# Kernel optimization log

Measured on AMD Instinct MI355X. Metric: run time of the kernel, lower is better.

Reference implementation:

```python
import jax, jax.numpy as jnp
import numpy as np

EMBED = 1024
HEADS = 16
HEAD_DIM = EMBED // HEADS
FFN = 4096
BSZ = 2
CHUNK = 128
NCHUNK = 16
REG_LEN = CHUNK * NCHUNK   # 2048
SUM_LEN = NCHUNK           # 1 summary token per chunk
NEG = -1e9


def _layer_norm(x, g, b, eps=1e-5):
    mu = x.mean(-1, keepdims=True)
    var = ((x - mu) ** 2).mean(-1, keepdims=True)
    return (x - mu) * jax.lax.rsqrt(var + eps) * g + b


def _build_mask(reg_chunk_ranges, sum_len, reg_len):
    # True = attention allowed. Museformer hierarchical scheme:
    #   rr: reg token attends reg tokens of its OWN chunk, causally
    #   rs: reg token attends summary tokens of STRICTLY EARLIER chunks
    #   sr: summary token of chunk c attends reg tokens of chunk c
    #   ss: causal among summary tokens
    bsz = reg_chunk_ranges.shape[0]
    starts = reg_chunk_ranges[:, :, 0]                       # [B, C]
    t = jnp.arange(reg_len)
    chunk_id = (t[None, :, None] >= starts[:, None, :]).sum(-1) - 1   # [B, R]
    sum_chunk = jnp.arange(sum_len)                          # [S]
    rr = (chunk_id[:, :, None] == chunk_id[:, None, :]) & (t[None, :, None] >= t[None, None, :])
    rs = sum_chunk[None, None, :] < chunk_id[:, :, None]     # [B, R, S]
    sr = chunk_id[:, None, :] == sum_chunk[None, :, None]    # [B, S, R]
    ss = jnp.broadcast_to(sum_chunk[:, None] >= sum_chunk[None, :], (bsz, sum_len, sum_len))
    top = jnp.concatenate([ss, sr], axis=2)
    bot = jnp.concatenate([rs, rr], axis=2)
    return jnp.concatenate([top, bot], axis=1)               # [B, S+R, S+R]


def _forward(x, w_q, w_k, w_v, w_o,
             ln_sa_sum_g, ln_sa_sum_b, ln_sa_reg_g, ln_sa_reg_b,
             sum_fc1_w, sum_fc1_b, sum_fc2_w, sum_fc2_b,
             reg_fc1_w, reg_fc1_b, reg_fc2_w, reg_fc2_b,
             ln_f_sum_g, ln_f_sum_b, ln_f_reg_g, ln_f_reg_b,
             reg_chunk_ranges, sum_len, reg_len):
    bsz, total, d = x.shape
    # --- self-attention block (pre-norm, separate LN for sum/reg parts) ---
    hs = _layer_norm(x[:, :sum_len], ln_sa_sum_g, ln_sa_sum_b)
    hr = _layer_norm(x[:, sum_len:], ln_sa_reg_g, ln_sa_reg_b)
    h = jnp.concatenate([hs, hr], axis=1)
    q = (h @ w_q.T).reshape(bsz, total, HEADS, HEAD_DIM)
    k = (h @ w_k.T).reshape(bsz, total, HEADS, HEAD_DIM)
    v = (h @ w_v.T).reshape(bsz, total, HEADS, HEAD_DIM)
    scores = jnp.einsum('bqhd,bkhd->bhqk', q, k) * (HEAD_DIM ** -0.5)
    mask = _build_mask(reg_chunk_ranges, sum_len, reg_len)   # [B, T, T] bool
    scores = jnp.where(mask[:, None], scores, NEG)
    attn = jax.nn.softmax(scores, axis=-1)
    ctx = jnp.einsum('bhqk,bkhd->bqhd', attn, v).reshape(bsz, total, d)
    x = x + ctx @ w_o.T
    # --- FFN block (pre-norm, separate LN/FFN for sum/reg parts) ---
    fs = _layer_norm(x[:, :sum_len], ln_f_sum_g, ln_f_sum_b)
    fs = jax.nn.relu(fs @ sum_fc1_w.T + sum_fc1_b) @ sum_fc2_w.T + sum_fc2_b
    fr = _layer_norm(x[:, sum_len:], ln_f_reg_g, ln_f_reg_b)
    fr = jax.nn.relu(fr @ reg_fc1_w.T + reg_fc1_b) @ reg_fc2_w.T + reg_fc2_b
    return x + jnp.concatenate([fs, fr], axis=1)


def setup_inputs() -> dict:
    key = jax.random.key(0)
    ks = jax.random.split(key, 12)
    s = 0.02
    total = SUM_LEN + REG_LEN
    starts = (np.arange(NCHUNK) * CHUNK).astype(np.int32)
    ranges = np.stack([starts, starts + CHUNK], axis=-1)     # [C, 2]
    reg_chunk_ranges = jnp.asarray(np.broadcast_to(ranges, (BSZ, NCHUNK, 2)).copy())
    d = dict(
        x=jax.random.normal(ks[0], (BSZ, total, EMBED), jnp.float32),
        w_q=jax.random.normal(ks[1], (EMBED, EMBED), jnp.float32) * s,
        w_k=jax.random.normal(ks[2], (EMBED, EMBED), jnp.float32) * s,
        w_v=jax.random.normal(ks[3], (EMBED, EMBED), jnp.float32) * s,
        w_o=jax.random.normal(ks[4], (EMBED, EMBED), jnp.float32) * s,
        ln_sa_sum_g=jnp.ones((EMBED,)), ln_sa_sum_b=jnp.zeros((EMBED,)),
        ln_sa_reg_g=jnp.ones((EMBED,)), ln_sa_reg_b=jnp.zeros((EMBED,)),
        sum_fc1_w=jax.random.normal(ks[5], (FFN, EMBED), jnp.float32) * s,
        sum_fc1_b=jnp.zeros((FFN,)),
        sum_fc2_w=jax.random.normal(ks[6], (EMBED, FFN), jnp.float32) * s,
        sum_fc2_b=jnp.zeros((EMBED,)),
        reg_fc1_w=jax.random.normal(ks[7], (FFN, EMBED), jnp.float32) * s,
        reg_fc1_b=jnp.zeros((FFN,)),
        reg_fc2_w=jax.random.normal(ks[8], (EMBED, FFN), jnp.float32) * s,
        reg_fc2_b=jnp.zeros((EMBED,)),
        ln_f_sum_g=jnp.ones((EMBED,)), ln_f_sum_b=jnp.zeros((EMBED,)),
        ln_f_reg_g=jnp.ones((EMBED,)), ln_f_reg_b=jnp.zeros((EMBED,)),
        reg_chunk_ranges=reg_chunk_ranges,
        sum_len=SUM_LEN,
        reg_len=REG_LEN,
    )
    return d


def reference(x, w_q, w_k, w_v, w_o,
              ln_sa_sum_g, ln_sa_sum_b, ln_sa_reg_g, ln_sa_reg_b,
              sum_fc1_w, sum_fc1_b, sum_fc2_w, sum_fc2_b,
              reg_fc1_w, reg_fc1_b, reg_fc2_w, reg_fc2_b,
              ln_f_sum_g, ln_f_sum_b, ln_f_reg_g, ln_f_reg_b,
              reg_chunk_ranges, sum_len, reg_len):
    return _forward(x, w_q, w_k, w_v, w_o,
                    ln_sa_sum_g, ln_sa_sum_b, ln_sa_reg_g, ln_sa_reg_b,
                    sum_fc1_w, sum_fc1_b, sum_fc2_w, sum_fc2_b,
                    reg_fc1_w, reg_fc1_b, reg_fc2_w, reg_fc2_b,
                    ln_f_sum_g, ln_f_sum_b, ln_f_reg_g, ln_f_reg_b,
                    reg_chunk_ranges, sum_len, reg_len)
```

## Files before the change

kernel.cpp:

```cpp
#include <hip/hip_runtime.h>
#include <stdint.h>

typedef __attribute__((ext_vector_type(8))) short short8;
typedef __attribute__((ext_vector_type(4))) float f32x4;

__device__ __forceinline__ float bf2f(short s) {
    union { unsigned u; float f; } c;
    c.u = ((unsigned)(unsigned short)s) << 16;
    return c.f;
}
__device__ __forceinline__ short f2bf(float f) {
    union { float f; unsigned u; } c; c.f = f;
    unsigned u = c.u + 0x7fffu + ((c.u >> 16) & 1u);
    return (short)(u >> 16);
}
__device__ __forceinline__ void gll16(const short* g, short* l) {
    __builtin_amdgcn_global_load_lds(
        (const __attribute__((address_space(1))) unsigned int*)g,
        (__attribute__((address_space(3))) unsigned int*)l, 16, 0, 0);
}

__global__ __launch_bounds__(256) void cvt_w(
    const float* __restrict__ wq, const float* __restrict__ wk,
    const float* __restrict__ wv, const float* __restrict__ wo,
    const float* __restrict__ f1s, const float* __restrict__ f2s,
    const float* __restrict__ f1r, const float* __restrict__ f2r,
    short* __restrict__ dst)
{
    size_t i = ((size_t)blockIdx.x * 256 + threadIdx.x) * 4;
    const float* src; size_t off;
    if (i < 4194304) {
        int seg = (int)(i >> 20);
        src = seg == 0 ? wq : seg == 1 ? wk : seg == 2 ? wv : wo;
        off = i & 1048575;
    } else {
        size_t ii = i - 4194304;
        int seg = (int)(ii >> 22);
        src = seg == 0 ? f1s : seg == 1 ? f2s : seg == 2 ? f1r : f2r;
        off = ii & 4194303;
    }
    float4 v = *(const float4*)(src + off);
    short4 o;
    o.x = f2bf(v.x); o.y = f2bf(v.y); o.z = f2bf(v.z); o.w = f2bf(v.w);
    *(short4*)(dst + i) = o;
}

template<int PHASE>
__global__ __launch_bounds__(256) void ln_k(
    const float* __restrict__ xin,
    const float* __restrict__ g_sum, const float* __restrict__ b_sum,
    const float* __restrict__ g_reg, const float* __restrict__ b_reg,
    short* __restrict__ out_all, short* __restrict__ out_s, short* __restrict__ out_r)
{
    int row = blockIdx.x;
    int b = row / 2064, t = row - b * 2064;
    int tid = threadIdx.x;
    const float* xr = xin + (size_t)row * 1024;
    float4 v = *(const float4*)(xr + tid * 4);
    float s = v.x + v.y + v.z + v.w;
#pragma unroll
    for (int off = 1; off < 64; off <<= 1) s += __shfl_xor(s, off);
    __shared__ float red[8];
    if ((tid & 63) == 0) red[tid >> 6] = s;
    __syncthreads();
    float mu = (red[0] + red[1] + red[2] + red[3]) * (1.0f / 1024.0f);
    float a0 = v.x - mu, a1 = v.y - mu, a2 = v.z - mu, a3 = v.w - mu;
    float qq = a0 * a0 + a1 * a1 + a2 * a2 + a3 * a3;
#pragma unroll
    for (int off = 1; off < 64; off <<= 1) qq += __shfl_xor(qq, off);
    if ((tid & 63) == 0) red[4 + (tid >> 6)] = qq;
    __syncthreads();
    float var = (red[4] + red[5] + red[6] + red[7]) * (1.0f / 1024.0f);
    float rs = rsqrtf(var + 1e-5f);
    const float* g  = (t < 16) ? g_sum : g_reg;
    const float* be = (t < 16) ? b_sum : b_reg;
    int c = tid * 4;
    short4 o;
    o.x = f2bf(a0 * rs * g[c]     + be[c]);
    o.y = f2bf(a1 * rs * g[c + 1] + be[c + 1]);
    o.z = f2bf(a2 * rs * g[c + 2] + be[c + 2]);
    o.w = f2bf(a3 * rs * g[c + 3] + be[c + 3]);
    short* dst;
    if (PHASE == 0) dst = out_all + (size_t)row * 1024;
    else dst = (t < 16) ? (out_s + ((size_t)b * 16 + t) * 1024)
                        : (out_r + ((size_t)b * 2048 + (t - 16)) * 1024);
    *(short4*)(dst + c) = o;
}

template<int MODE>
__global__ __launch_bounds__(256) void gemm_bt(
    const short* __restrict__ A, int M, int K, int klen,
    const short* __restrict__ B0, const short* __restrict__ B1, const short* __restrict__ B2,
    const float* __restrict__ bias,
    void* __restrict__ o0, void* __restrict__ o1, void* __restrict__ o2, int seg)
{
    const int tid = threadIdx.x;
    const int w = tid >> 6, l = tid & 63;
    const int lr = l & 15, lh = l >> 4;
    const int m0 = blockIdx.x * 128;
    int ntile = blockIdx.y, nsel = 0;
    const short* B = B0;
    if (MODE == 0) { nsel = ntile >> 3; ntile &= 7; B = nsel == 0 ? B0 : (nsel == 1 ? B1 : B2); }
    const int n0 = ntile * 128;
    const int wr = (w >> 1) * 64, wc = (w & 1) * 64;
    const int kbase = blockIdx.z * klen;

    __shared__ __align__(16) short As[128 * 32];
    __shared__ __align__(16) short Bs[128 * 32];

    const int srow = w * 32 + (l >> 2);
    const int scol = (l & 3) * 8;
    int ar0 = m0 + srow;      if (ar0 > M - 1) ar0 = M - 1;
    int ar1 = m0 + srow + 16; if (ar1 > M - 1) ar1 = M - 1;
    const short* ga0 = A + (size_t)ar0 * K + scol;
    const short* ga1 = A + (size_t)ar1 * K + scol;
    const short* gb0 = B + (size_t)(n0 + srow) * K + scol;
    const short* gb1 = B + (size_t)(n0 + srow + 16) * K + scol;
    short* la0 = As + (w * 32) * 32;
    short* la1 = As + (w * 32 + 16) * 32;
    short* lb0 = Bs + (w * 32) * 32;
    short* lb1 = Bs + (w * 32 + 16) * 32;

    f32x4 acc[4][4];
#pragma unroll
    for (int m = 0; m < 4; ++m)
#pragma unroll
        for (int n = 0; n < 4; ++n) acc[m][n] = (f32x4){0.f, 0.f, 0.f, 0.f};

    for (int k0 = kbase; k0 < kbase + klen; k0 += 32) {
        gll16(ga0 + k0, la0);
        gll16(ga1 + k0, la1);
        gll16(gb0 + k0, lb0);
        gll16(gb1 + k0, lb1);
        __syncthreads();
        short8 af[4], bfr[4];
#pragma unroll
        for (int m = 0; m < 4; ++m)
            af[m] = *(const short8*)(As + (wr + m * 16 + lr) * 32 + lh * 8);
#pragma unroll
        for (int n = 0; n < 4; ++n)
            bfr[n] = *(const short8*)(Bs + (wc + n * 16 + lr) * 32 + lh * 8);
#pragma unroll
        for (int m = 0; m < 4; ++m)
#pragma unroll
            for (int n = 0; n < 4; ++n)
                acc[m][n] = __builtin_amdgcn_mfma_f32_16x16x32_bf16(af[m], bfr[n], acc[m][n], 0, 0, 0);
        __syncthreads();
    }

#pragma unroll
    for (int m = 0; m < 4; ++m) {
#pragma unroll
        for (int n = 0; n < 4; ++n) {
            int gc = n0 + wc + n * 16 + lr;
#pragma unroll
            for (int j = 0; j < 4; ++j) {
                int gr = m0 + wr + m * 16 + lh * 4 + j;
                if (gr >= M) continue;
                float val = acc[m][n][j];
                if (MODE == 0) {
                    short* o = (short*)(nsel == 0 ? o0 : (nsel == 1 ? o1 : o2));
                    o[(size_t)gr * 1024 + gc] = f2bf(val);
                } else if (MODE == 1) {
                    float* P = (float*)o0 + (size_t)blockIdx.z * (size_t)seg;
                    P[(size_t)gr * 1024 + gc] = val;
                } else {
                    val += bias[gc];
                    val = val > 0.f ? val : 0.f;
                    ((short*)o0)[(size_t)gr * 4096 + gc] = f2bf(val);
                }
            }
        }
    }
}

__global__ __launch_bounds__(256) void reduce_wo(
    const float* __restrict__ x, const float* __restrict__ P, float* __restrict__ x1)
{
    size_t i = ((size_t)blockIdx.x * 256 + threadIdx.x) * 4;
    float4 a  = *(const float4*)(x + i);
    float4 p0 = *(const float4*)(P + i);
    float4 p1 = *(const float4*)(P + i + 4227072);
    float4 o;
    o.x = a.x + p0.x + p1.x; o.y = a.y + p0.y + p1.y;
    o.z = a.z + p0.z + p1.z; o.w = a.w + p0.w + p1.w;
    *(float4*)(x1 + i) = o;
}

__global__ __launch_bounds__(256) void reduce_f2reg(
    const float* __restrict__ x1, const float* __restrict__ P,
    const float* __restrict__ bias, float* __restrict__ out)
{
    size_t i = ((size_t)blockIdx.x * 256 + threadIdx.x) * 4;
    int gr = (int)(i >> 10), c = (int)(i & 1023);
    size_t g = (size_t)((gr >> 11) * 2064 + 16 + (gr & 2047)) * 1024 + c;
    float4 p0 = *(const float4*)(P + i);
    float4 p1 = *(const float4*)(P + i + 4194304);
    float4 r  = *(const float4*)(x1 + g);
    float4 bb = *(const float4*)(bias + c);
    float4 o;
    o.x = r.x + p0.x + p1.x + bb.x; o.y = r.y + p0.y + p1.y + bb.y;
    o.z = r.z + p0.z + p1.z + bb.z; o.w = r.w + p0.w + p1.w + bb.w;
    *(float4*)(out + g) = o;
}

__global__ __launch_bounds__(256) void reduce_f2sum(
    const float* __restrict__ x1, const float* __restrict__ P,
    const float* __restrict__ bias, float* __restrict__ out)
{
    int i = (blockIdx.x * 256 + threadIdx.x) * 4;
    int gr = i >> 10, c = i & 1023;
    size_t g = (size_t)((gr >> 4) * 2064 + (gr & 15)) * 1024 + c;
    float4 r  = *(const float4*)(x1 + g);
    float4 bb = *(const float4*)(bias + c);
    float ox = r.x + bb.x, oy = r.y + bb.y, oz = r.z + bb.z, ow = r.w + bb.w;
#pragma unroll
    for (int s = 0; s < 16; ++s) {
        float4 p = *(const float4*)(P + s * 32768 + i);
        ox += p.x; oy += p.y; oz += p.z; ow += p.w;
    }
    float4 o; o.x = ox; o.y = oy; o.z = oz; o.w = ow;
    *(float4*)(out + g) = o;
}

__global__ __launch_bounds__(256) void attn_reg(
    const short* __restrict__ q, const short* __restrict__ k,
    const short* __restrict__ v, short* __restrict__ ctx)
{
    __shared__ __align__(16) short Pl[128 * 168];
    __shared__ __align__(16) short Vt[64 * 168];
    short* Kl = Pl;

    const int tid = threadIdx.x;
    const int w = tid >> 6, l = tid & 63, lr = l & 15, lh = l >> 4;
    const int c = blockIdx.x, h = blockIdx.y, b = blockIdx.z;
    const int hc = h * 64;
    const size_t rowq0 = (size_t)b * 2064 + 16 + (size_t)c * 128;

    for (int ch = tid; ch < 1152; ch += 256) {
        int row = ch >> 3, kk = (ch & 7) << 3;
        size_t grow = (row < 16) ? ((size_t)b * 2064 + row) : (rowq0 + row - 16);
        *(int4*)(Kl + row * 72 + kk) = *(const int4*)(k + grow * 1024 + hc + kk);
    }
    for (int ch = tid; ch < 1152; ch += 256) {
        int j = ch % 144, db = ch / 144;
        size_t grow = (j < 16) ? ((size_t)b * 2064 + j) : (rowq0 + j - 16);
        short8 dv = *(const short8*)(v + grow * 1024 + hc + db * 8);
#pragma unroll
        for (int i = 0; i < 8; ++i) Vt[(db * 8 + i) * 168 + j] = dv[i];
    }
    for (int idx = tid; idx < 1024; idx += 256) {
        int d = idx >> 4, jj = 144 + (idx & 15);
        Vt[d * 168 + jj] = 0;
    }
    __syncthreads();

    short8 qf[2][2];
#pragma unroll
    for (int m = 0; m < 2; ++m) {
        size_t grow = rowq0 + w * 32 + m * 16 + lr;
#pragma unroll
        for (int ks = 0; ks < 2; ++ks)
            qf[m][ks] = *(const short8*)(q + grow * 1024 + hc + ks * 32 + lh * 8);
    }

    f32x4 s[2][9];
#pragma unroll
    for (int m = 0; m < 2; ++m)
#pragma unroll
        for (int n = 0; n < 9; ++n) s[m][n] = (f32x4){0.f, 0.f, 0.f, 0.f};
#pragma unroll
    for (int n = 0; n < 9; ++n) {
        const short* kr = Kl + (n * 16 + lr) * 72;
        short8 k0 = *(const short8*)(kr + lh * 8);
        short8 k1 = *(const short8*)(kr + 32 + lh * 8);
        s[0][n] = __builtin_amdgcn_mfma_f32_16x16x32_bf16(qf[0][0], k0, s[0][n], 0, 0, 0);
        s[0][n] = __builtin_amdgcn_mfma_f32_16x16x32_bf16(qf[0][1], k1, s[0][n], 0, 0, 0);
        s[1][n] = __builtin_amdgcn_mfma_f32_16x16x32_bf16(qf[1][0], k0, s[1][n], 0, 0, 0);
        s[1][n] = __builtin_amdgcn_mfma_f32_16x16x32_bf16(qf[1][1], k1, s[1][n], 0, 0, 0);
    }

    float inv_[2][4];
#pragma unroll
    for (int m = 0; m < 2; ++m) {
#pragma unroll
        for (int j = 0; j < 4; ++j) {
            int p = w * 32 + m * 16 + lh * 4 + j;
            float best = -1e30f;
            float e[9];
#pragma unroll
            for (int n = 0; n < 9; ++n) {
                int kk = n * 16 + lr;
                bool vis = (kk < 16) ? (kk < c) : (kk - 16 <= p);
                float val = vis ? s[m][n][j] * 0.125f : -1e30f;
                e[n] = val;
                best = fmaxf(best, val);
            }
#pragma unroll
            for (int off = 1; off < 16; off <<= 1) best = fmaxf(best, __shfl_xor(best, off));
            float sm = 0.f;
#pragma unroll
            for (int n = 0; n < 9; ++n) {
                float ex = __expf(e[n] - best);
                s[m][n][j] = ex;
                sm += ex;
            }
#pragma unroll
            for (int off = 1; off < 16; off <<= 1) sm += __shfl_xor(sm, off);
            inv_[m][j] = 1.0f / sm;
        }
    }

    __syncthreads();
#pragma unroll
    for (int m = 0; m < 2; ++m)
#pragma unroll
        for (int n = 0; n < 9; ++n)
#pragma unroll
            for (int j = 0; j < 4; ++j)
                Pl[(w * 32 + m * 16 + lh * 4 + j) * 168 + n * 16 + lr] = f2bf(s[m][n][j]);
    for (int idx = l; idx < 512; idx += 64) {
        int rr = idx >> 4, kkp = 144 + (idx & 15);
        Pl[(w * 32 + rr) * 168 + kkp] = 0;
    }
    __syncthreads();

    f32x4 dacc[2][4];
#pragma unroll
    for (int m = 0; m < 2; ++m)
#pragma unroll
        for (int n = 0; n < 4; ++n) dacc[m][n] = (f32x4){0.f, 0.f, 0.f, 0.f};
#pragma unroll
    for (int ks = 0; ks < 5; ++ks) {
        int kk0 = ks * 32;
        short8 pa[2];
#pragma unroll
        for (int m = 0; m < 2; ++m)
            pa[m] = *(const short8*)(Pl + (w * 32 + m * 16 + lr) * 168 + kk0 + lh * 8);
#pragma unroll
        for (int n = 0; n < 4; ++n) {
            short8 vb = *(const short8*)(Vt + (n * 16 + lr) * 168 + kk0 + lh * 8);
            dacc[0][n] = __builtin_amdgcn_mfma_f32_16x16x32_bf16(pa[0], vb, dacc[0][n], 0, 0, 0);
            dacc[1][n] = __builtin_amdgcn_mfma_f32_16x16x32_bf16(pa[1], vb, dacc[1][n], 0, 0, 0);
        }
    }

#pragma unroll
    for (int m = 0; m < 2; ++m)
#pragma unroll
        for (int n = 0; n < 4; ++n)
#pragma unroll
            for (int j = 0; j < 4; ++j) {
                int p = w * 32 + m * 16 + lh * 4 + j;
                ctx[(rowq0 + p) * 1024 + hc + n * 16 + lr] = f2bf(dacc[m][n][j] * inv_[m][j]);
            }
}

__global__ __launch_bounds__(64) void attn_sum(
    const short* __restrict__ q, const short* __restrict__ k,
    const short* __restrict__ v, short* __restrict__ ctx)
{
    int idx = blockIdx.x;
    int b = idx >> 8, h = (idx >> 4) & 15, s = idx & 15;
    int l = threadIdx.x;
    int hc = h * 64;
    size_t qrow = (size_t)b * 2064 + s;
    __shared__ float qv[64];
    __shared__ float pp[192];
    qv[l] = bf2f(q[qrow * 1024 + hc + l]);
    __syncthreads();
    float sc[3];
#pragma unroll
    for (int i = 0; i < 3; ++i) {
        int j = l + i * 64;
        float t = -1e30f;
        if (j < 144 && (j >= 16 || j <= s)) {
            size_t kr = (j < 16) ? ((size_t)b * 2064 + j)
                                 : ((size_t)b * 2064 + 16 + (size_t)s * 128 + (j - 16));
            const short* kp = k + kr * 1024 + hc;
            float acc = 0.f;
            for (int d = 0; d < 64; ++d) acc += qv[d] * bf2f(kp[d]);
            t = acc * 0.125f;
        }
        sc[i] = t;
    }
    float mx = fmaxf(sc[0], fmaxf(sc[1], sc[2]));
#pragma unroll
    for (int off = 1; off < 64; off <<= 1) mx = fmaxf(mx, __shfl_xor(mx, off));
    float sm = 0.f;
#pragma unroll
    for (int i = 0; i < 3; ++i) {
        float ex = (sc[i] > -1e29f) ? __expf(sc[i] - mx) : 0.f;
        pp[l + i * 64] = ex;
        sm += ex;
    }
#pragma unroll
    for (int off = 1; off < 64; off <<= 1) sm += __shfl_xor(sm, off);
    __syncthreads();
    float invs = 1.0f / sm;
    float acc = 0.f;
    for (int j = 0; j < 144; ++j) {
        float pj = pp[j];
        size_t vr = (j < 16) ? ((size_t)b * 2064 + j)
                             : ((size_t)b * 2064 + 16 + (size_t)s * 128 + (j - 16));
        acc += pj * bf2f(v[vr * 1024 + hc + l]);
    }
    ctx[qrow * 1024 + hc + l] = f2bf(acc * invs);
}

extern "C" void kernel_launch(void* const* d_in, const int* in_sizes, int n_in,
                              void* d_out, int out_size, void* d_ws, size_t ws_size,
                              hipStream_t stream) {
    const float* x    = (const float*)d_in[0];
    const float* wq   = (const float*)d_in[1];
    const float* wk   = (const float*)d_in[2];
    const float* wv   = (const float*)d_in[3];
    const float* wo   = (const float*)d_in[4];
    const float* lsg  = (const float*)d_in[5];
    const float* lsb  = (const float*)d_in[6];
    const float* lrg  = (const float*)d_in[7];
    const float* lrb  = (const float*)d_in[8];
    const float* sf1w = (const float*)d_in[9];
    const float* sf1b = (const float*)d_in[10];
    const float* sf2w = (const float*)d_in[11];
    const float* sf2b = (const float*)d_in[12];
    const float* rf1w = (const float*)d_in[13];
    const float* rf1b = (const float*)d_in[14];
    const float* rf2w = (const float*)d_in[15];
    const float* rf2b = (const float*)d_in[16];
    const float* fsg  = (const float*)d_in[17];
    const float* fsb  = (const float*)d_in[18];
    const float* frg  = (const float*)d_in[19];
    const float* frb  = (const float*)d_in[20];
    float* out = (float*)d_out;

    char* ws = (char*)d_ws;
    short* wbf   = (short*)ws;
    short* wq_b  = wbf;
    short* wk_b  = wbf + 1048576;
    short* wv_b  = wbf + 2097152;
    short* wo_b  = wbf + 3145728;
    short* f1s_b = wbf + 4194304;
    short* f2s_b = wbf + 8388608;
    short* f1r_b = wbf + 12582912;
    short* f2r_b = wbf + 16777216;
    short* h_all  = (short*)(ws + 41943040);
    short* h2_reg = h_all;
    short* h2_sum = (short*)(ws + 41943040 + 8388608);
    float* Pwo    = (float*)(ws + 41943040);
    float* Psum   = (float*)(ws + 41943040);
    short* qb   = (short*)(ws + 50397184);
    short* kb   = qb + 4227072;
    short* vb   = kb + 4227072;
    short* ctxb = vb + 4227072;
    short* f1_reg = qb;
    short* f1_sum = qb + 16777216;
    float* Pf2 = (float*)ws;
    float* x1 = (float*)(ws + 84213760);

    cvt_w<<<20480, 256, 0, stream>>>(wq, wk, wv, wo, sf1w, sf2w, rf1w, rf2w, wbf);
    ln_k<0><<<4128, 256, 0, stream>>>(x, lsg, lsb, lrg, lrb, h_all, nullptr, nullptr);
    gemm_bt<0><<<dim3(33, 24, 1), 256, 0, stream>>>(h_all, 4128, 1024, 1024,
        wq_b, wk_b, wv_b, nullptr, qb, kb, vb, 0);
    attn_reg<<<dim3(16, 16, 2), 256, 0, stream>>>(qb, kb, vb, ctxb);
    attn_sum<<<512, 64, 0, stream>>>(qb, kb, vb, ctxb);
    gemm_bt<1><<<dim3(33, 8, 2), 256, 0, stream>>>(ctxb, 4128, 1024, 512,
        wo_b, nullptr, nullptr, nullptr, Pwo, nullptr, nullptr, 4227072);
    reduce_wo<<<4128, 256, 0, stream>>>(x, Pwo, x1);
    ln_k<1><<<4128, 256, 0, stream>>>(x1, fsg, fsb, frg, frb, nullptr, h2_sum, h2_reg);
    gemm_bt<2><<<dim3(32, 32, 1), 256, 0, stream>>>(h2_reg, 4096, 1024, 1024,
        f1r_b, nullptr, nullptr, rf1b, f1_reg, nullptr, nullptr, 0);
    gemm_bt<2><<<dim3(1, 32, 1), 256, 0, stream>>>(h2_sum, 32, 1024, 1024,
        f1s_b, nullptr, nullptr, sf1b, f1_sum, nullptr, nullptr, 0);
    gemm_bt<1><<<dim3(1, 8, 16), 256, 0, stream>>>(f1_sum, 32, 4096, 256,
        f2s_b, nullptr, nullptr, nullptr, Psum, nullptr, nullptr, 32768);
    reduce_f2sum<<<32, 256, 0, stream>>>(x1, Psum, sf2b, out);
    gemm_bt<1><<<dim3(32, 8, 2), 256, 0, stream>>>(f1_reg, 4096, 4096, 2048,
        f2r_b, nullptr, nullptr, nullptr, Pf2, nullptr, nullptr, 4194304);
    reduce_f2reg<<<4096, 256, 0, stream>>>(x1, Pf2, rf2b, out);
}
```

Measured before the change: 331.8 us.

## Double-buffer GEMM LDS tiles and fuse Wo reduction into second layer norm

The GEMM kernel now keeps two LDS buffers per operand and issues the global-to-LDS loads for the next K step before computing the current one. This removes one barrier per iteration and overlaps load latency with MFMA work. The residual add of the split-K Wo partials is folded into the second layer-norm kernel, which drops a separate elementwise pass, and workspace buffers are rearranged so the reused regions do not overlap. LDS use doubles, which may lower occupancy, and the new aliasing layout must stay free of read/write conflicts.

```diff
diff --git a/kernel.cpp b/kernel.cpp
--- a/kernel.cpp
+++ b/kernel.cpp
@@ -47,7 +47,7 @@
 
 template<int PHASE>
 __global__ __launch_bounds__(256) void ln_k(
-    const float* __restrict__ xin,
+    const float* __restrict__ xin, const float* __restrict__ P, float* __restrict__ x1out,
     const float* __restrict__ g_sum, const float* __restrict__ b_sum,
     const float* __restrict__ g_reg, const float* __restrict__ b_reg,
     short* __restrict__ out_all, short* __restrict__ out_s, short* __restrict__ out_r)
@@ -55,8 +55,16 @@
     int row = blockIdx.x;
     int b = row / 2064, t = row - b * 2064;
     int tid = threadIdx.x;
-    const float* xr = xin + (size_t)row * 1024;
-    float4 v = *(const float4*)(xr + tid * 4);
+    int c = tid * 4;
+    size_t base = (size_t)row * 1024 + c;
+    float4 v = *(const float4*)(xin + base);
+    if (PHASE == 1) {
+        float4 p0 = *(const float4*)(P + base);
+        float4 p1 = *(const float4*)(P + base + 4227072);
+        v.x += p0.x + p1.x; v.y += p0.y + p1.y;
+        v.z += p0.z + p1.z; v.w += p0.w + p1.w;
+        *(float4*)(x1out + base) = v;
+    }
     float s = v.x + v.y + v.z + v.w;
 #pragma unroll
     for (int off = 1; off < 64; off <<= 1) s += __shfl_xor(s, off);
@@ -74,7 +82,6 @@
     float rs = rsqrtf(var + 1e-5f);
     const float* g  = (t < 16) ? g_sum : g_reg;
     const float* be = (t < 16) ? b_sum : b_reg;
-    int c = tid * 4;
     short4 o;
     o.x = f2bf(a0 * rs * g[c]     + be[c]);
     o.y = f2bf(a1 * rs * g[c + 1] + be[c + 1]);
@@ -105,21 +112,18 @@
     const int wr = (w >> 1) * 64, wc = (w & 1) * 64;
     const int kbase = blockIdx.z * klen;
 
-    __shared__ __align__(16) short As[128 * 32];
-    __shared__ __align__(16) short Bs[128 * 32];
+    __shared__ __align__(16) short As[2 * 4096];
+    __shared__ __align__(16) short Bs[2 * 4096];
 
     const int srow = w * 32 + (l >> 2);
     const int scol = (l & 3) * 8;
     int ar0 = m0 + srow;      if (ar0 > M - 1) ar0 = M - 1;
     int ar1 = m0 + srow + 16; if (ar1 > M - 1) ar1 = M - 1;
-    const short* ga0 = A + (size_t)ar0 * K + scol;
-    const short* ga1 = A + (size_t)ar1 * K + scol;
-    const short* gb0 = B + (size_t)(n0 + srow) * K + scol;
-    const short* gb1 = B + (size_t)(n0 + srow + 16) * K + scol;
-    short* la0 = As + (w * 32) * 32;
-    short* la1 = As + (w * 32 + 16) * 32;
-    short* lb0 = Bs + (w * 32) * 32;
-    short* lb1 = Bs + (w * 32 + 16) * 32;
+    const short* ga0 = A + (size_t)ar0 * K + scol + kbase;
+    const short* ga1 = A + (size_t)ar1 * K + scol + kbase;
+    const short* gb0 = B + (size_t)(n0 + srow) * K + scol + kbase;
+    const short* gb1 = B + (size_t)(n0 + srow + 16) * K + scol + kbase;
+    const int lofs = (w * 32) * 32;
 
     f32x4 acc[4][4];
 #pragma unroll
@@ -127,25 +131,35 @@
 #pragma unroll
         for (int n = 0; n < 4; ++n) acc[m][n] = (f32x4){0.f, 0.f, 0.f, 0.f};
 
-    for (int k0 = kbase; k0 < kbase + klen; k0 += 32) {
-        gll16(ga0 + k0, la0);
-        gll16(ga1 + k0, la1);
-        gll16(gb0 + k0, lb0);
-        gll16(gb1 + k0, lb1);
+    gll16(ga0, As + lofs);
+    gll16(ga1, As + lofs + 512);
+    gll16(gb0, Bs + lofs);
+    gll16(gb1, Bs + lofs + 512);
+
+    const int nk = klen >> 5;
+    for (int t = 0; t < nk; ++t) {
         __syncthreads();
+        const int cur = (t & 1) << 12;
+        if (t + 1 < nk) {
+            const int nb = cur ^ 4096;
+            const int k0 = (t + 1) * 32;
+            gll16(ga0 + k0, As + nb + lofs);
+            gll16(ga1 + k0, As + nb + lofs + 512);
+            gll16(gb0 + k0, Bs + nb + lofs);
+            gll16(gb1 + k0, Bs + nb + lofs + 512);
+        }
         short8 af[4], bfr[4];
 #pragma unroll
         for (int m = 0; m < 4; ++m)
-            af[m] = *(const short8*)(As + (wr + m * 16 + lr) * 32 + lh * 8);
+            af[m] = *(const short8*)(As + cur + (wr + m * 16 + lr) * 32 + lh * 8);
 #pragma unroll
         for (int n = 0; n < 4; ++n)
-            bfr[n] = *(const short8*)(Bs + (wc + n * 16 + lr) * 32 + lh * 8);
+            bfr[n] = *(const short8*)(Bs + cur + (wc + n * 16 + lr) * 32 + lh * 8);
 #pragma unroll
         for (int m = 0; m < 4; ++m)
 #pragma unroll
             for (int n = 0; n < 4; ++n)
                 acc[m][n] = __builtin_amdgcn_mfma_f32_16x16x32_bf16(af[m], bfr[n], acc[m][n], 0, 0, 0);
-        __syncthreads();
     }
 
 #pragma unroll
@@ -172,19 +186,6 @@
             }
         }
     }
-}
-
-__global__ __launch_bounds__(256) void reduce_wo(
-    const float* __restrict__ x, const float* __restrict__ P, float* __restrict__ x1)
-{
-    size_t i = ((size_t)blockIdx.x * 256 + threadIdx.x) * 4;
-    float4 a  = *(const float4*)(x + i);
-    float4 p0 = *(const float4*)(P + i);
-    float4 p1 = *(const float4*)(P + i + 4227072);
-    float4 o;
-    o.x = a.x + p0.x + p1.x; o.y = a.y + p0.y + p1.y;
-    o.z = a.z + p0.z + p1.z; o.w = a.w + p0.w + p1.w;
-    *(float4*)(x1 + i) = o;
 }
 
 __global__ __launch_bounds__(256) void reduce_f2reg(
@@ -444,30 +445,31 @@
     short* f2s_b = wbf + 8388608;
     short* f1r_b = wbf + 12582912;
     short* f2r_b = wbf + 16777216;
-    short* h_all  = (short*)(ws + 41943040);
-    short* h2_reg = h_all;
-    short* h2_sum = (short*)(ws + 41943040 + 8388608);
-    float* Pwo    = (float*)(ws + 41943040);
-    float* Psum   = (float*)(ws + 41943040);
+    short* h_all = (short*)(ws + 41943040);
     short* qb   = (short*)(ws + 50397184);
     short* kb   = qb + 4227072;
     short* vb   = kb + 4227072;
     short* ctxb = vb + 4227072;
-    short* f1_reg = qb;
-    short* f1_sum = qb + 16777216;
+    float* Pwo = (float*)(ws + 41943040);
+    float* x1 = (float*)(ws + 84213760);
+    short* h2_reg = (short*)ws;
+    short* h2_sum = (short*)(ws + 75759616);
+    short* f1_reg = (short*)(ws + 41943040);
+    short* f1_sum = (short*)(ws + 75825152);
+    float* Psum = (float*)(ws + 8388608);
     float* Pf2 = (float*)ws;
-    float* x1 = (float*)(ws + 84213760);
 
     cvt_w<<<20480, 256, 0, stream>>>(wq, wk, wv, wo, sf1w, sf2w, rf1w, rf2w, wbf);
-    ln_k<0><<<4128, 256, 0, stream>>>(x, lsg, lsb, lrg, lrb, h_all, nullptr, nullptr);
+    ln_k<0><<<4128, 256, 0, stream>>>(x, nullptr, nullptr, lsg, lsb, lrg, lrb,
+                                      h_all, nullptr, nullptr);
     gemm_bt<0><<<dim3(33, 24, 1), 256, 0, stream>>>(h_all, 4128, 1024, 1024,
         wq_b, wk_b, wv_b, nullptr, qb, kb, vb, 0);
     attn_reg<<<dim3(16, 16, 2), 256, 0, stream>>>(qb, kb, vb, ctxb);
     attn_sum<<<512, 64, 0, stream>>>(qb, kb, vb, ctxb);
     gemm_bt<1><<<dim3(33, 8, 2), 256, 0, stream>>>(ctxb, 4128, 1024, 512,
         wo_b, nullptr, nullptr, nullptr, Pwo, nullptr, nullptr, 4227072);
-    reduce_wo<<<4128, 256, 0, stream>>>(x, Pwo, x1);
-    ln_k<1><<<4128, 256, 0, stream>>>(x1, fsg, fsb, frg, frb, nullptr, h2_sum, h2_reg);
+    ln_k<1><<<4128, 256, 0, stream>>>(x, Pwo, x1, fsg, fsb, frg, frb,
+                                      nullptr, h2_sum, h2_reg);
     gemm_bt<2><<<dim3(32, 32, 1), 256, 0, stream>>>(h2_reg, 4096, 1024, 1024,
         f1r_b, nullptr, nullptr, rf1b, f1_reg, nullptr, nullptr, 0);
     gemm_bt<2><<<dim3(1, 32, 1), 256, 0, stream>>>(h2_sum, 32, 1024, 1024,
```

After: 302.7 us. 1.1x faster.
